# Kernel tuning notes

Hardware: AMD Instinct MI355X
Metric: run time of the kernel (lower is better)

Reference implementation:

```python
import jax, jax.numpy as jnp
import numpy as np

D_MODEL = 768
NUM_HEADS = 12
D_HEAD = D_MODEL // NUM_HEADS


def setup_inputs() -> dict:
    key = jax.random.key(0)
    ks = jax.random.split(key, 11)
    B, S = 1, 4096
    s = 1.0 / np.sqrt(D_MODEL)
    inp = {
        'q': jax.random.normal(ks[0], (B, S, D_MODEL), dtype=jnp.float32),
        'k': jax.random.normal(ks[1], (B, S, D_MODEL), dtype=jnp.float32),
        'v': jax.random.normal(ks[2], (B, S, D_MODEL), dtype=jnp.float32),
        'wq': jax.random.normal(ks[3], (D_MODEL, D_MODEL), dtype=jnp.float32) * s,
        'bq': jnp.zeros((D_MODEL,), dtype=jnp.float32),
        'wk': jax.random.normal(ks[4], (D_MODEL, D_MODEL), dtype=jnp.float32) * s,
        'bk': jnp.zeros((D_MODEL,), dtype=jnp.float32),
        'wv': jax.random.normal(ks[5], (D_MODEL, D_MODEL), dtype=jnp.float32) * s,
        'bv': jnp.zeros((D_MODEL,), dtype=jnp.float32),
        'wo': jax.random.normal(ks[6], (D_MODEL, D_MODEL), dtype=jnp.float32) * s,
        'bo': jnp.zeros((D_MODEL,), dtype=jnp.float32),
    }
    return inp


def reference(q, k, v, wq, bq, wk, bk, wv, bv, wo, bo):
    B, S, _ = q.shape
    # linear projections (torch Linear: x @ W^T + b)
    qh = (q @ wq.T + bq).reshape(B, S, NUM_HEADS, D_HEAD).transpose(0, 2, 1, 3)
    kh = (k @ wk.T + bk).reshape(B, S, NUM_HEADS, D_HEAD).transpose(0, 2, 1, 3)
    vh = (v @ wv.T + bv).reshape(B, S, NUM_HEADS, D_HEAD).transpose(0, 2, 1, 3)
    scores = jnp.einsum('bhqd,bhkd->bhqk', qh, kh) / jnp.sqrt(jnp.float32(D_HEAD))
    causal = jnp.tril(jnp.ones((S, S), dtype=bool))  # [S,S] causal mask
    scores = jnp.where(causal, scores, jnp.finfo(scores.dtype).min)
    attn = jax.nn.softmax(scores, axis=-1)  # dropout omitted (eval mode)
    out = jnp.einsum('bhqk,bhkd->bhqd', attn, vh)
    out = out.transpose(0, 2, 1, 3).reshape(B, S, D_MODEL)
    return out @ wo.T + bo
```

## Files before the change

kernel.cpp:

```cpp
#include <hip/hip_runtime.h>
#include <stdint.h>

typedef __attribute__((ext_vector_type(8))) short short8;
typedef __attribute__((ext_vector_type(2))) float float2v;
typedef __attribute__((ext_vector_type(4))) float float4v;
typedef __attribute__((ext_vector_type(16))) float f32x16;
typedef __attribute__((ext_vector_type(2))) uint32_t uint32x2;
typedef __attribute__((ext_vector_type(4))) uint32_t uint32x4;
typedef __attribute__((ext_vector_type(2))) unsigned int uint2v;

__device__ __forceinline__ uint32_t pkbf(float a, float b) {
  uint32_t r;
  asm("v_cvt_pk_bf16_f32 %0, %1, %2" : "=v"(r) : "v"(a), "v"(b));
  return r;
}

__device__ __forceinline__ float2v pkadd(float2v a, float2v b) {
  float2v d;
  asm("v_pk_add_f32 %0, %1, %2" : "=v"(d) : "v"(a), "v"(b));
  return d;
}

__device__ __forceinline__ float fexp2(float x) {
#if __has_builtin(__builtin_amdgcn_exp2f)
  return __builtin_amdgcn_exp2f(x);
#else
  return exp2f(x);
#endif
}

__device__ __forceinline__ uint2v plswap(uint32_t a, uint32_t b) {
#if __has_builtin(__builtin_amdgcn_permlane32_swap)
  return __builtin_amdgcn_permlane32_swap(a, b, false, false);
#else
  asm("v_permlane32_swap_b32 %0, %1" : "+v"(a), "+v"(b));
  uint2v r;
  r[0] = a;
  r[1] = b;
  return r;
#endif
}

__device__ __forceinline__ void gll16(const unsigned short* g, unsigned short* l) {
  __builtin_amdgcn_global_load_lds(
      (const __attribute__((address_space(1))) void*)g,
      (__attribute__((address_space(3))) void*)l, 16, 0, 0);
}

__device__ __forceinline__ void cvt_cell(const float* src, unsigned short* dst) {
  const float4v a0 = *(const float4v*)src;
  const float4v a1 = *(const float4v*)(src + 4);
  uint32x4 w;
  w[0] = pkbf(a0[0], a0[1]);
  w[1] = pkbf(a0[2], a0[3]);
  w[2] = pkbf(a1[0], a1[1]);
  w[3] = pkbf(a1[2], a1[3]);
  *(uint32x4*)dst = w;
}

__global__ __launch_bounds__(256) void gemm_qkv(
    const float* __restrict__ xq, const float* __restrict__ xk,
    const float* __restrict__ xv,
    const float* __restrict__ wq, const float* __restrict__ wk,
    const float* __restrict__ wv,
    const float* __restrict__ bq, const float* __restrict__ bk,
    const float* __restrict__ bv,
    unsigned short* __restrict__ Qp, unsigned short* __restrict__ Kp,
    unsigned short* __restrict__ Vt, float qscale)
{
  __shared__ unsigned short As[64 * 64];
  __shared__ unsigned short Ws[128 * 64];
  const int z = blockIdx.z;
  const float* A = z == 0 ? xq : z == 1 ? xk : xv;
  const float* W = z == 0 ? wq : z == 1 ? wk : wv;
  const float* bias = z == 0 ? bq : z == 1 ? bk : bv;
  const int M = 4096, N = 768, K = 768;
  const int tid = threadIdx.x, wave = tid >> 6, lane = tid & 63;
  const int g = lane >> 4, l16 = lane & 15;
  const int sw = l16 & 7;
  const int m0 = blockIdx.x * 64, n0 = blockIdx.y * 128;
  const int wm = (wave & 1) * 32, wn = (wave >> 1) * 64;
  const int r8 = lane >> 3, skg = lane & 7;

  float4v acc[4][2] = {};

  for (int k0 = 0; k0 < K; k0 += 64) {
    if (k0) __syncthreads();
    #pragma unroll
    for (int cc = 0; cc < 2; ++cc) {
      const int row = wave * 16 + cc * 8 + r8;
      const int kg = skg ^ (row & 7);
      cvt_cell(A + (size_t)(m0 + row) * K + k0 + kg * 8, &As[row * 64 + skg * 8]);
    }
    #pragma unroll
    for (int cc = 0; cc < 4; ++cc) {
      const int row = wave * 32 + cc * 8 + r8;
      const int kg = skg ^ (row & 7);
      cvt_cell(W + (size_t)(n0 + row) * K + k0 + kg * 8, &Ws[row * 64 + skg * 8]);
    }
    __syncthreads();
    #pragma unroll
    for (int kk = 0; kk < 2; ++kk) {
      const int kg = ((kk * 4 + g) ^ sw) * 8;
      short8 xf[2], wf[4];
      #pragma unroll
      for (int t = 0; t < 2; ++t) xf[t] = *(const short8*)&As[(wm + t * 16 + l16) * 64 + kg];
      #pragma unroll
      for (int t = 0; t < 4; ++t) wf[t] = *(const short8*)&Ws[(wn + t * 16 + l16) * 64 + kg];
      if (z < 2) {
        #pragma unroll
        for (int i = 0; i < 4; ++i)
          #pragma unroll
          for (int j = 0; j < 2; ++j)
            acc[i][j] = __builtin_amdgcn_mfma_f32_16x16x32_bf16(wf[i], xf[j], acc[i][j], 0, 0, 0);
      } else {
        #pragma unroll
        for (int b = 0; b < 4; ++b)
          #pragma unroll
          for (int a2 = 0; a2 < 2; ++a2)
            acc[b][a2] = __builtin_amdgcn_mfma_f32_16x16x32_bf16(xf[a2], wf[b], acc[b][a2], 0, 0, 0);
      }
    }
  }

  if (z < 2) {
    unsigned short* O = z == 0 ? Qp : Kp;
    const float osc = z == 0 ? qscale : 1.0f;
    #pragma unroll
    for (int i = 0; i < 4; ++i) {
      const int nb = n0 + wn + i * 16 + 4 * g;
      const float4v bb = *(const float4v*)&bias[nb];
      #pragma unroll
      for (int j = 0; j < 2; ++j) {
        const int m = m0 + wm + j * 16 + l16;
        uint32x2 pk;
        pk[0] = pkbf((acc[i][j][0] + bb[0]) * osc, (acc[i][j][1] + bb[1]) * osc);
        pk[1] = pkbf((acc[i][j][2] + bb[2]) * osc, (acc[i][j][3] + bb[3]) * osc);
        *(uint32x2*)(O + (size_t)m * N + nb) = pk;
      }
    }
  } else {
    #pragma unroll
    for (int b = 0; b < 4; ++b) {
      const int n = n0 + wn + b * 16 + l16;
      const float bb = bias[n];
      #pragma unroll
      for (int a2 = 0; a2 < 2; ++a2) {
        const int mb = m0 + wm + a2 * 16 + 4 * g;
        uint32x2 pk;
        pk[0] = pkbf(acc[b][a2][0] + bb, acc[b][a2][1] + bb);
        pk[1] = pkbf(acc[b][a2][2] + bb, acc[b][a2][3] + bb);
        *(uint32x2*)(Vt + (size_t)n * M + mb) = pk;
      }
    }
  }
}

__global__ __launch_bounds__(256, 4) void flash_part(
    const unsigned short* __restrict__ Qp,
    const unsigned short* __restrict__ Kp,
    const unsigned short* __restrict__ Vt,
    unsigned short* __restrict__ Opart,
    float* __restrict__ lpart)
{
  __shared__ unsigned short lds_k[2][64 * 64];
  __shared__ unsigned short lds_v[2][64 * 64];
  const int S = 4096, DM = 768;

  const int gid = blockIdx.x;
  const int h = gid % 12;
  const int e = 79 - gid / 12;
  int t, c;
  if (e < 8)       { t = e;                c = 0; }
  else if (e < 24) { t = 8 + (e - 8) / 2;  c = (e - 8) % 2; }
  else if (e < 48) { t = 16 + (e - 24) / 3; c = (e - 24) % 3; }
  else             { t = 24 + (e - 48) / 4; c = (e - 48) % 4; }
  const int kb0 = c * 16;
  const int kbe = min(kb0 + 16, 2 * t + 2);

  const int tid = threadIdx.x, wave = tid >> 6, lane = tid & 63;
  const int l31 = lane & 31, hi = lane >> 5, sw7 = lane & 7;
  const int qbase = t * 128 + wave * 32;
  const int qrow = qbase + l31;

  short8 qf[4];
  {
    const unsigned short* qp = Qp + (size_t)qrow * DM + h * 64 + hi * 8;
    qf[0] = *(const short8*)(qp);
    qf[1] = *(const short8*)(qp + 16);
    qf[2] = *(const short8*)(qp + 32);
    qf[3] = *(const short8*)(qp + 48);
  }

  f32x16 o0 = {}, o1 = {};
  float2v lsA = {0.f, 0.f}, lsB = {0.f, 0.f};

  const int strow = wave * 16 + (lane >> 3);
  const int skg = lane & 7;

  #pragma unroll
  for (int cc = 0; cc < 2; ++cc) {
    const int row = strow + cc * 8;
    const int kg = skg ^ (row & 7);
    gll16(Kp + (size_t)(kb0 * 64 + row) * DM + h * 64 + kg * 8,
          &lds_k[0][(wave * 16 + cc * 8) * 64]);
    gll16(Vt + (size_t)(h * 64 + row) * S + kb0 * 64 + kg * 8,
          &lds_v[0][(wave * 16 + cc * 8) * 64]);
  }
  __syncthreads();

  for (int kb = kb0; kb < kbe; ++kb) {
    const int cur = kb & 1;
    if (kb + 1 < kbe) {
      const int nb = cur ^ 1;
      #pragma unroll
      for (int cc = 0; cc < 2; ++cc) {
        const int row = strow + cc * 8;
        const int kg = skg ^ (row & 7);
        gll16(Kp + (size_t)((kb + 1) * 64 + row) * DM + h * 64 + kg * 8,
              &lds_k[nb][(wave * 16 + cc * 8) * 64]);
        gll16(Vt + (size_t)(h * 64 + row) * S + (kb + 1) * 64 + kg * 8,
              &lds_v[nb][(wave * 16 + cc * 8) * 64]);
      }
    }
    const unsigned short* kc = lds_k[cur];
    const unsigned short* vc = lds_v[cur];

    f32x16 s0 = {}, s1 = {};
    __builtin_amdgcn_s_setprio(1);
    #pragma unroll
    for (int d4 = 0; d4 < 4; ++d4) {
      const int cg = ((2 * d4 + hi) ^ sw7) * 8;
      short8 ka = *(const short8*)&kc[l31 * 64 + cg];
      short8 kb2 = *(const short8*)&kc[(32 + l31) * 64 + cg];
      s0 = __builtin_amdgcn_mfma_f32_32x32x16_bf16(ka, qf[d4], s0, 0, 0, 0);
      s1 = __builtin_amdgcn_mfma_f32_32x32x16_bf16(kb2, qf[d4], s1, 0, 0, 0);
    }
    __builtin_amdgcn_s_setprio(0);

    const bool diag = (kb + 1) * 64 > qbase;
    short8 pb[4];
    auto sm_pack = [&](const f32x16& sv, int ks, short8* pbp) {
      #pragma unroll
      for (int jh = 0; jh < 2; ++jh) {
        float pe[8];
        if (diag) {
          #pragma unroll
          for (int rr = 0; rr < 8; ++rr) {
            const int key = kb * 64 + ks + (rr & 3) + 8 * (2 * jh + (rr >> 2)) + 4 * hi;
            pe[rr] = fexp2(key <= qrow ? sv[jh * 8 + rr] : -1e30f);
          }
        } else {
          #pragma unroll
          for (int rr = 0; rr < 8; ++rr) pe[rr] = fexp2(sv[jh * 8 + rr]);
        }
        float2v p01 = {pe[0], pe[1]}, p23 = {pe[2], pe[3]};
        float2v p45 = {pe[4], pe[5]}, p67 = {pe[6], pe[7]};
        lsA = pkadd(lsA, pkadd(p01, p45));
        lsB = pkadd(lsB, pkadd(p23, p67));
        const uint32_t x01 = pkbf(pe[0], pe[1]);
        const uint32_t x23 = pkbf(pe[2], pe[3]);
        const uint32_t y01 = pkbf(pe[4], pe[5]);
        const uint32_t y23 = pkbf(pe[6], pe[7]);
        uint2v r01 = plswap(x01, y01);
        uint2v r23 = plswap(x23, y23);
        union { uint32x4 u; short8 s; } w;
        w.u[0] = r01[0];
        w.u[1] = r23[0];
        w.u[2] = r01[1];
        w.u[3] = r23[1];
        pbp[jh] = w.s;
      }
    };
    sm_pack(s0, 0, &pb[0]);
    sm_pack(s1, 32, &pb[2]);

    __builtin_amdgcn_s_setprio(1);
    #pragma unroll
    for (int kk = 0; kk < 4; ++kk) {
      const int cg = ((2 * kk + hi) ^ sw7) * 8;
      short8 va0 = *(const short8*)&vc[l31 * 64 + cg];
      short8 va1 = *(const short8*)&vc[(32 + l31) * 64 + cg];
      o0 = __builtin_amdgcn_mfma_f32_32x32x16_bf16(va0, pb[kk], o0, 0, 0, 0);
      o1 = __builtin_amdgcn_mfma_f32_32x32x16_bf16(va1, pb[kk], o1, 0, 0, 0);
    }
    __builtin_amdgcn_s_setprio(0);

    __syncthreads();
  }

  float L = (lsA[0] + lsA[1]) + (lsB[0] + lsB[1]);
  L += __shfl_xor(L, 32);
  const int slot = (h * 32 + t) * 4 + c;
  if (hi == 0) lpart[slot * 128 + wave * 32 + l31] = L;
  unsigned short* ob = Opart + (size_t)slot * 8192 + (size_t)(wave * 32 + l31) * 64;
  #pragma unroll
  for (int dt = 0; dt < 2; ++dt) {
    const f32x16& oo = dt ? o1 : o0;
    #pragma unroll
    for (int a = 0; a < 4; ++a) {
      uint32x2 ov;
      ov[0] = pkbf(oo[4 * a + 0], oo[4 * a + 1]);
      ov[1] = pkbf(oo[4 * a + 2], oo[4 * a + 3]);
      *(uint32x2*)(ob + dt * 32 + 8 * a + 4 * hi) = ov;
    }
  }
}

__global__ __launch_bounds__(256) void flash_combine(
    const unsigned short* __restrict__ Opart, const float* __restrict__ lpart,
    unsigned short* __restrict__ AO)
{
  const int t2 = blockIdx.x, h = blockIdx.y;
  const int t = t2 >> 1;
  const int nc = (2 * t + 17) >> 4;
  const int slot0 = (h * 32 + t) * 4;
  const int tid = threadIdx.x;
  const int qr = tid >> 2, dc = (tid & 3) * 16;
  const int ql = (t2 & 1) * 64 + qr;
  float acc[16];
  #pragma unroll
  for (int j = 0; j < 16; ++j) acc[j] = 0.0f;
  float lsum = 0.0f;
  for (int cc = 0; cc < nc; ++cc) {
    const int slot = slot0 + cc;
    lsum += lpart[slot * 128 + ql];
    const uint32x4* p = (const uint32x4*)(Opart + (size_t)slot * 8192 + ql * 64 + dc);
    uint32x4 w0 = p[0], w1 = p[1];
    #pragma unroll
    for (int j = 0; j < 4; ++j) {
      union { uint32_t u; float f; } lo, hi;
      lo.u = w0[j] << 16; hi.u = w0[j] & 0xffff0000u;
      acc[2 * j] += lo.f; acc[2 * j + 1] += hi.f;
      lo.u = w1[j] << 16; hi.u = w1[j] & 0xffff0000u;
      acc[8 + 2 * j] += lo.f; acc[8 + 2 * j + 1] += hi.f;
    }
  }
  const float inv = 1.0f / lsum;
  uint32x4 o0, o1;
  #pragma unroll
  for (int j = 0; j < 4; ++j) {
    o0[j] = pkbf(acc[2 * j] * inv, acc[2 * j + 1] * inv);
    o1[j] = pkbf(acc[8 + 2 * j] * inv, acc[8 + 2 * j + 1] * inv);
  }
  unsigned short* dst = AO + (size_t)(t * 128 + ql) * 768 + h * 64 + dc;
  *(uint32x4*)dst = o0;
  *(uint32x4*)(dst + 8) = o1;
}

__global__ __launch_bounds__(256) void gemm_out(
    const unsigned short* __restrict__ A, const float* __restrict__ W,
    const float* __restrict__ bias, float* __restrict__ Out)
{
  __shared__ unsigned short As[64 * 64];
  __shared__ unsigned short Ws[64 * 64];
  const int N = 768, K = 768;
  const int tid = threadIdx.x, wave = tid >> 6, lane = tid & 63;
  const int g = lane >> 4, l16 = lane & 15;
  const int sw = l16 & 7;
  const int m0 = blockIdx.x * 64, n0 = blockIdx.y * 64;
  const int wm = (wave & 1) * 32, wn = (wave >> 1) * 32;
  const int r8 = lane >> 3, skg = lane & 7;

  float4v acc[2][2] = {};

  for (int k0 = 0; k0 < K; k0 += 64) {
    if (k0) __syncthreads();
    #pragma unroll
    for (int cc = 0; cc < 2; ++cc) {
      const int row = wave * 16 + cc * 8 + r8;
      const int kg = skg ^ (row & 7);
      gll16(A + (size_t)(m0 + row) * K + k0 + kg * 8, &As[(wave * 16 + cc * 8) * 64]);
    }
    #pragma unroll
    for (int cc = 0; cc < 2; ++cc) {
      const int row = wave * 16 + cc * 8 + r8;
      const int kg = skg ^ (row & 7);
      cvt_cell(W + (size_t)(n0 + row) * K + k0 + kg * 8, &Ws[row * 64 + skg * 8]);
    }
    __syncthreads();
    #pragma unroll
    for (int kk = 0; kk < 2; ++kk) {
      const int kg = ((kk * 4 + g) ^ sw) * 8;
      short8 xf[2], wf[2];
      #pragma unroll
      for (int t = 0; t < 2; ++t) {
        xf[t] = *(const short8*)&As[(wm + t * 16 + l16) * 64 + kg];
        wf[t] = *(const short8*)&Ws[(wn + t * 16 + l16) * 64 + kg];
      }
      #pragma unroll
      for (int i = 0; i < 2; ++i)
        #pragma unroll
        for (int j = 0; j < 2; ++j)
          acc[i][j] = __builtin_amdgcn_mfma_f32_16x16x32_bf16(wf[i], xf[j], acc[i][j], 0, 0, 0);
    }
  }

  #pragma unroll
  for (int i = 0; i < 2; ++i) {
    const int nb = n0 + wn + i * 16 + 4 * g;
    const float4v bb = *(const float4v*)&bias[nb];
    #pragma unroll
    for (int j = 0; j < 2; ++j) {
      const int m = m0 + wm + j * 16 + l16;
      float4v ov;
      #pragma unroll
      for (int rr = 0; rr < 4; ++rr) ov[rr] = acc[i][j][rr] + bb[rr];
      *(float4v*)(Out + (size_t)m * N + nb) = ov;
    }
  }
}

extern "C" void kernel_launch(void* const* d_in, const int* in_sizes, int n_in,
                              void* d_out, int out_size, void* d_ws, size_t ws_size,
                              hipStream_t stream) {
  const float* q  = (const float*)d_in[0];
  const float* k  = (const float*)d_in[1];
  const float* v  = (const float*)d_in[2];
  const float* wq = (const float*)d_in[3];
  const float* bq = (const float*)d_in[4];
  const float* wk = (const float*)d_in[5];
  const float* bk = (const float*)d_in[6];
  const float* wv = (const float*)d_in[7];
  const float* bv = (const float*)d_in[8];
  const float* wo = (const float*)d_in[9];
  const float* bo = (const float*)d_in[10];
  float* out = (float*)d_out;

  const int S = 4096, D = 768;
  unsigned short* Qp    = (unsigned short*)d_ws;
  unsigned short* Kp    = Qp  + (size_t)S * D;
  unsigned short* Vt    = Kp  + (size_t)S * D;
  unsigned short* AO    = Vt  + (size_t)S * D;
  unsigned short* Opart = AO  + (size_t)S * D;
  float*          lpart = (float*)(Opart + (size_t)1536 * 8192);

  const float SC = 0.125f * 1.44269504089f;
  dim3 blk(256);
  gemm_qkv<<<dim3(64, 6, 3), blk, 0, stream>>>(q, k, v, wq, wk, wv,
                                               bq, bk, bv, Qp, Kp, Vt, SC);
  flash_part<<<dim3(960), blk, 0, stream>>>(Qp, Kp, Vt, Opart, lpart);
  flash_combine<<<dim3(64, 12), blk, 0, stream>>>(Opart, lpart, AO);
  gemm_out<<<dim3(64, 12), blk, 0, stream>>>(AO, wo, bo, out);
}
```

Before: 195.7 us.

## Prefetch next K-slab into registers during MFMA in projection GEMMs

In both the QKV projection GEMM and the output projection GEMM, the fp32 global loads for the next 64-wide K slab are now issued into registers before the MFMA loop on the current slab. The converted bf16 data is written to LDS only after compute finishes. This is meant to hide global load latency behind the matrix math instead of stalling at the start of each iteration. In exchange it uses more registers per thread (up to 24 extra float4 values in gemm_qkv), which may lower occupancy, and each iteration keeps two barriers.

```diff
diff --git a/kernel.cpp b/kernel.cpp
--- a/kernel.cpp
+++ b/kernel.cpp
@@ -47,9 +47,8 @@
       (__attribute__((address_space(3))) void*)l, 16, 0, 0);
 }
 
-__device__ __forceinline__ void cvt_cell(const float* src, unsigned short* dst) {
-  const float4v a0 = *(const float4v*)src;
-  const float4v a1 = *(const float4v*)(src + 4);
+__device__ __forceinline__ void pack_cell(const float4v& a0, const float4v& a1,
+                                          unsigned short* dst) {
   uint32x4 w;
   w[0] = pkbf(a0[0], a0[1]);
   w[1] = pkbf(a0[2], a0[3]);
@@ -82,23 +81,45 @@
   const int wm = (wave & 1) * 32, wn = (wave >> 1) * 64;
   const int r8 = lane >> 3, skg = lane & 7;
 
+  int arow[2], akg[2], wrow[4], wkg[4];
+  #pragma unroll
+  for (int cc = 0; cc < 2; ++cc) { arow[cc] = wave * 16 + cc * 8 + r8; akg[cc] = skg ^ (arow[cc] & 7); }
+  #pragma unroll
+  for (int cc = 0; cc < 4; ++cc) { wrow[cc] = wave * 32 + cc * 8 + r8; wkg[cc] = skg ^ (wrow[cc] & 7); }
+
+  float4v ra[2][2], rw[4][2];
+  auto loadSlab = [&](int k0) {
+    #pragma unroll
+    for (int cc = 0; cc < 2; ++cc) {
+      const float* s = A + (size_t)(m0 + arow[cc]) * K + k0 + akg[cc] * 8;
+      ra[cc][0] = *(const float4v*)s;
+      ra[cc][1] = *(const float4v*)(s + 4);
+    }
+    #pragma unroll
+    for (int cc = 0; cc < 4; ++cc) {
+      const float* s = W + (size_t)(n0 + wrow[cc]) * K + k0 + wkg[cc] * 8;
+      rw[cc][0] = *(const float4v*)s;
+      rw[cc][1] = *(const float4v*)(s + 4);
+    }
+  };
+  auto writeSlab = [&]() {
+    #pragma unroll
+    for (int cc = 0; cc < 2; ++cc)
+      pack_cell(ra[cc][0], ra[cc][1], &As[arow[cc] * 64 + skg * 8]);
+    #pragma unroll
+    for (int cc = 0; cc < 4; ++cc)
+      pack_cell(rw[cc][0], rw[cc][1], &Ws[wrow[cc] * 64 + skg * 8]);
+  };
+
   float4v acc[4][2] = {};
 
+  loadSlab(0);
+  writeSlab();
+  __syncthreads();
+
   for (int k0 = 0; k0 < K; k0 += 64) {
-    if (k0) __syncthreads();
-    #pragma unroll
-    for (int cc = 0; cc < 2; ++cc) {
-      const int row = wave * 16 + cc * 8 + r8;
-      const int kg = skg ^ (row & 7);
-      cvt_cell(A + (size_t)(m0 + row) * K + k0 + kg * 8, &As[row * 64 + skg * 8]);
-    }
-    #pragma unroll
-    for (int cc = 0; cc < 4; ++cc) {
-      const int row = wave * 32 + cc * 8 + r8;
-      const int kg = skg ^ (row & 7);
-      cvt_cell(W + (size_t)(n0 + row) * K + k0 + kg * 8, &Ws[row * 64 + skg * 8]);
-    }
-    __syncthreads();
+    const bool more = (k0 + 64 < K);
+    if (more) loadSlab(k0 + 64);
     #pragma unroll
     for (int kk = 0; kk < 2; ++kk) {
       const int kg = ((kk * 4 + g) ^ sw) * 8;
@@ -120,6 +141,11 @@
           for (int a2 = 0; a2 < 2; ++a2)
             acc[b][a2] = __builtin_amdgcn_mfma_f32_16x16x32_bf16(xf[a2], wf[b], acc[b][a2], 0, 0, 0);
       }
+    }
+    if (more) {
+      __syncthreads();
+      writeSlab();
+      __syncthreads();
     }
   }
 
@@ -362,23 +388,41 @@
   const int wm = (wave & 1) * 32, wn = (wave >> 1) * 32;
   const int r8 = lane >> 3, skg = lane & 7;
 
+  int srow[2], skgx[2];
+  #pragma unroll
+  for (int cc = 0; cc < 2; ++cc) { srow[cc] = wave * 16 + cc * 8 + r8; skgx[cc] = skg ^ (srow[cc] & 7); }
+
+  float4v rwv[2][2];
+  auto loadW = [&](int k0) {
+    #pragma unroll
+    for (int cc = 0; cc < 2; ++cc) {
+      const float* s = W + (size_t)(n0 + srow[cc]) * K + k0 + skgx[cc] * 8;
+      rwv[cc][0] = *(const float4v*)s;
+      rwv[cc][1] = *(const float4v*)(s + 4);
+    }
+  };
+  auto writeW = [&]() {
+    #pragma unroll
+    for (int cc = 0; cc < 2; ++cc)
+      pack_cell(rwv[cc][0], rwv[cc][1], &Ws[srow[cc] * 64 + skg * 8]);
+  };
+  auto dmaA = [&](int k0) {
+    #pragma unroll
+    for (int cc = 0; cc < 2; ++cc)
+      gll16(A + (size_t)(m0 + srow[cc]) * K + k0 + skgx[cc] * 8,
+            &As[(wave * 16 + cc * 8) * 64]);
+  };
+
   float4v acc[2][2] = {};
 
+  loadW(0);
+  dmaA(0);
+  writeW();
+  __syncthreads();
+
   for (int k0 = 0; k0 < K; k0 += 64) {
-    if (k0) __syncthreads();
-    #pragma unroll
-    for (int cc = 0; cc < 2; ++cc) {
-      const int row = wave * 16 + cc * 8 + r8;
-      const int kg = skg ^ (row & 7);
-      gll16(A + (size_t)(m0 + row) * K + k0 + kg * 8, &As[(wave * 16 + cc * 8) * 64]);
-    }
-    #pragma unroll
-    for (int cc = 0; cc < 2; ++cc) {
-      const int row = wave * 16 + cc * 8 + r8;
-      const int kg = skg ^ (row & 7);
-      cvt_cell(W + (size_t)(n0 + row) * K + k0 + kg * 8, &Ws[row * 64 + skg * 8]);
-    }
-    __syncthreads();
+    const bool more = (k0 + 64 < K);
+    if (more) loadW(k0 + 64);
     #pragma unroll
     for (int kk = 0; kk < 2; ++kk) {
       const int kg = ((kk * 4 + g) ^ sw) * 8;
@@ -393,6 +437,12 @@
         #pragma unroll
         for (int j = 0; j < 2; ++j)
           acc[i][j] = __builtin_amdgcn_mfma_f32_16x16x32_bf16(wf[i], xf[j], acc[i][j], 0, 0, 0);
+    }
+    if (more) {
+      __syncthreads();
+      dmaA(k0 + 64);
+      writeW();
+      __syncthreads();
     }
   }
 
```

After: 198.4 us. About the same (+1.4%).

## Load fp32 tiles directly to LDS and convert to bf16 at fragment read

Applied to the files above, without the earlier changes.

Replaces the register-staged fp32-to-bf16 conversion on the global-to-LDS path with direct global_load_lds of fp32 data into swizzled LDS tiles. The bf16 packing now happens when MFMA fragments are read from LDS. gemm_qkv also shrinks its N tile from 128 to 64 to fit the doubled LDS footprint, which doubles its grid. The aim is to cut VGPR staging and load latency, at the cost of more LDS traffic, repeated conversions per fragment read, and less reuse per block.

```diff
diff --git a/kernel.cpp b/kernel.cpp
--- a/kernel.cpp
+++ b/kernel.cpp
@@ -47,15 +47,10 @@
       (__attribute__((address_space(3))) void*)l, 16, 0, 0);
 }
 
-__device__ __forceinline__ void cvt_cell(const float* src, unsigned short* dst) {
-  const float4v a0 = *(const float4v*)src;
-  const float4v a1 = *(const float4v*)(src + 4);
-  uint32x4 w;
-  w[0] = pkbf(a0[0], a0[1]);
-  w[1] = pkbf(a0[2], a0[3]);
-  w[2] = pkbf(a1[0], a1[1]);
-  w[3] = pkbf(a1[2], a1[3]);
-  *(uint32x4*)dst = w;
+__device__ __forceinline__ void gll16f(const float* g, float* l) {
+  __builtin_amdgcn_global_load_lds(
+      (const __attribute__((address_space(1))) void*)g,
+      (__attribute__((address_space(3))) void*)l, 16, 0, 0);
 }
 
 __global__ __launch_bounds__(256) void gemm_qkv(
@@ -68,8 +63,8 @@
     unsigned short* __restrict__ Qp, unsigned short* __restrict__ Kp,
     unsigned short* __restrict__ Vt, float qscale)
 {
-  __shared__ unsigned short As[64 * 64];
-  __shared__ unsigned short Ws[128 * 64];
+  __shared__ float Asf[64 * 64];
+  __shared__ float Wsf[64 * 64];
   const int z = blockIdx.z;
   const float* A = z == 0 ? xq : z == 1 ? xk : xv;
   const float* W = z == 0 ? wq : z == 1 ? wk : wv;
@@ -77,45 +72,53 @@
   const int M = 4096, N = 768, K = 768;
   const int tid = threadIdx.x, wave = tid >> 6, lane = tid & 63;
   const int g = lane >> 4, l16 = lane & 15;
-  const int sw = l16 & 7;
-  const int m0 = blockIdx.x * 64, n0 = blockIdx.y * 128;
-  const int wm = (wave & 1) * 32, wn = (wave >> 1) * 64;
-  const int r8 = lane >> 3, skg = lane & 7;
-
-  float4v acc[4][2] = {};
+  const int m0 = blockIdx.x * 64, n0 = blockIdx.y * 64;
+  const int wm = (wave & 1) * 32, wn = (wave >> 1) * 32;
+
+  auto f32frag = [&](const float* lds, int row, int gg) -> short8 {
+    const int s = row & 15;
+    const float4v a = *(const float4v*)&lds[row * 64 + (((2 * gg) ^ s) << 2)];
+    const float4v b = *(const float4v*)&lds[row * 64 + (((2 * gg + 1) ^ s) << 2)];
+    union { uint32x4 u; short8 sv; } w;
+    w.u[0] = pkbf(a[0], a[1]);
+    w.u[1] = pkbf(a[2], a[3]);
+    w.u[2] = pkbf(b[0], b[1]);
+    w.u[3] = pkbf(b[2], b[3]);
+    return w.sv;
+  };
+
+  float4v acc[2][2] = {};
 
   for (int k0 = 0; k0 < K; k0 += 64) {
     if (k0) __syncthreads();
     #pragma unroll
-    for (int cc = 0; cc < 2; ++cc) {
-      const int row = wave * 16 + cc * 8 + r8;
-      const int kg = skg ^ (row & 7);
-      cvt_cell(A + (size_t)(m0 + row) * K + k0 + kg * 8, &As[row * 64 + skg * 8]);
-    }
-    #pragma unroll
-    for (int cc = 0; cc < 4; ++cc) {
-      const int row = wave * 32 + cc * 8 + r8;
-      const int kg = skg ^ (row & 7);
-      cvt_cell(W + (size_t)(n0 + row) * K + k0 + kg * 8, &Ws[row * 64 + skg * 8]);
+    for (int rr = 0; rr < 4; ++rr) {
+      const int row = rr * 16 + wave * 4 + (lane >> 4);
+      const int cl = (lane & 15) ^ (row & 15);
+      gll16f(A + (size_t)(m0 + row) * K + k0 + cl * 4,
+             &Asf[(rr * 16 + wave * 4) * 64]);
+      gll16f(W + (size_t)(n0 + row) * K + k0 + cl * 4,
+             &Wsf[(rr * 16 + wave * 4) * 64]);
     }
     __syncthreads();
     #pragma unroll
     for (int kk = 0; kk < 2; ++kk) {
-      const int kg = ((kk * 4 + g) ^ sw) * 8;
-      short8 xf[2], wf[4];
-      #pragma unroll
-      for (int t = 0; t < 2; ++t) xf[t] = *(const short8*)&As[(wm + t * 16 + l16) * 64 + kg];
-      #pragma unroll
-      for (int t = 0; t < 4; ++t) wf[t] = *(const short8*)&Ws[(wn + t * 16 + l16) * 64 + kg];
+      const int gg = kk * 4 + g;
+      short8 xf[2], wf[2];
+      #pragma unroll
+      for (int t = 0; t < 2; ++t) {
+        xf[t] = f32frag(Asf, wm + t * 16 + l16, gg);
+        wf[t] = f32frag(Wsf, wn + t * 16 + l16, gg);
+      }
       if (z < 2) {
         #pragma unroll
-        for (int i = 0; i < 4; ++i)
+        for (int i = 0; i < 2; ++i)
           #pragma unroll
           for (int j = 0; j < 2; ++j)
             acc[i][j] = __builtin_amdgcn_mfma_f32_16x16x32_bf16(wf[i], xf[j], acc[i][j], 0, 0, 0);
       } else {
         #pragma unroll
-        for (int b = 0; b < 4; ++b)
+        for (int b = 0; b < 2; ++b)
           #pragma unroll
           for (int a2 = 0; a2 < 2; ++a2)
             acc[b][a2] = __builtin_amdgcn_mfma_f32_16x16x32_bf16(xf[a2], wf[b], acc[b][a2], 0, 0, 0);
@@ -127,7 +130,7 @@
     unsigned short* O = z == 0 ? Qp : Kp;
     const float osc = z == 0 ? qscale : 1.0f;
     #pragma unroll
-    for (int i = 0; i < 4; ++i) {
+    for (int i = 0; i < 2; ++i) {
       const int nb = n0 + wn + i * 16 + 4 * g;
       const float4v bb = *(const float4v*)&bias[nb];
       #pragma unroll
@@ -141,7 +144,7 @@
     }
   } else {
     #pragma unroll
-    for (int b = 0; b < 4; ++b) {
+    for (int b = 0; b < 2; ++b) {
       const int n = n0 + wn + b * 16 + l16;
       const float bb = bias[n];
       #pragma unroll
@@ -353,7 +356,7 @@
     const float* __restrict__ bias, float* __restrict__ Out)
 {
   __shared__ unsigned short As[64 * 64];
-  __shared__ unsigned short Ws[64 * 64];
+  __shared__ float Wsf[64 * 64];
   const int N = 768, K = 768;
   const int tid = threadIdx.x, wave = tid >> 6, lane = tid & 63;
   const int g = lane >> 4, l16 = lane & 15;
@@ -362,6 +365,18 @@
   const int wm = (wave & 1) * 32, wn = (wave >> 1) * 32;
   const int r8 = lane >> 3, skg = lane & 7;
 
+  auto f32frag = [&](const float* lds, int row, int gg) -> short8 {
+    const int s = row & 15;
+    const float4v a = *(const float4v*)&lds[row * 64 + (((2 * gg) ^ s) << 2)];
+    const float4v b = *(const float4v*)&lds[row * 64 + (((2 * gg + 1) ^ s) << 2)];
+    union { uint32x4 u; short8 sv; } w;
+    w.u[0] = pkbf(a[0], a[1]);
+    w.u[1] = pkbf(a[2], a[3]);
+    w.u[2] = pkbf(b[0], b[1]);
+    w.u[3] = pkbf(b[2], b[3]);
+    return w.sv;
+  };
+
   float4v acc[2][2] = {};
 
   for (int k0 = 0; k0 < K; k0 += 64) {
@@ -373,20 +388,22 @@
       gll16(A + (size_t)(m0 + row) * K + k0 + kg * 8, &As[(wave * 16 + cc * 8) * 64]);
     }
     #pragma unroll
-    for (int cc = 0; cc < 2; ++cc) {
-      const int row = wave * 16 + cc * 8 + r8;
-      const int kg = skg ^ (row & 7);
-      cvt_cell(W + (size_t)(n0 + row) * K + k0 + kg * 8, &Ws[row * 64 + skg * 8]);
+    for (int rr = 0; rr < 4; ++rr) {
+      const int row = rr * 16 + wave * 4 + (lane >> 4);
+      const int cl = (lane & 15) ^ (row & 15);
+      gll16f(W + (size_t)(n0 + row) * K + k0 + cl * 4,
+             &Wsf[(rr * 16 + wave * 4) * 64]);
     }
     __syncthreads();
     #pragma unroll
     for (int kk = 0; kk < 2; ++kk) {
       const int kg = ((kk * 4 + g) ^ sw) * 8;
+      const int gg = kk * 4 + g;
       short8 xf[2], wf[2];
       #pragma unroll
       for (int t = 0; t < 2; ++t) {
         xf[t] = *(const short8*)&As[(wm + t * 16 + l16) * 64 + kg];
-        wf[t] = *(const short8*)&Ws[(wn + t * 16 + l16) * 64 + kg];
+        wf[t] = f32frag(Wsf, wn + t * 16 + l16, gg);
       }
       #pragma unroll
       for (int i = 0; i < 2; ++i)
@@ -437,8 +454,8 @@
 
   const float SC = 0.125f * 1.44269504089f;
   dim3 blk(256);
-  gemm_qkv<<<dim3(64, 6, 3), blk, 0, stream>>>(q, k, v, wq, wk, wv,
-                                               bq, bk, bv, Qp, Kp, Vt, SC);
+  gemm_qkv<<<dim3(64, 12, 3), blk, 0, stream>>>(q, k, v, wq, wk, wv,
+                                                bq, bk, bv, Qp, Kp, Vt, SC);
   flash_part<<<dim3(960), blk, 0, stream>>>(Qp, Kp, Vt, Opart, lpart);
   flash_combine<<<dim3(64, 12), blk, 0, stream>>>(Opart, lpart, AO);
   gemm_out<<<dim3(64, 12), blk, 0, stream>>>(AO, wo, bo, out);
```

Measured after the change: 198.6 us. No clear change (+1.5%).
